# Performance work log

Measured on AMD Instinct MI355X. Metric: run time of the kernel, lower is better.

Reference implementation:

```python
import jax, jax.numpy as jnp
import numpy as np

B, T, C = 8, 2048, 1024
EXP = 4
EPS = 1e-6


def rmsnorm(x, w):
    xf = x.astype(jnp.float32)
    y = xf * jax.lax.rsqrt(jnp.mean(xf * xf, axis=-1, keepdims=True) + EPS)
    return y.astype(x.dtype) * w


def setup_inputs() -> dict:
    key = jax.random.key(0)
    ks = jax.random.split(key, 8)
    x = jax.random.normal(ks[0], (B, T, C), dtype=jnp.float32)
    norm1_w = jnp.ones((C,), jnp.float32)
    norm2_w = jnp.ones((C,), jnp.float32)
    s1 = 1.0 / np.sqrt(C)
    s2 = 1.0 / np.sqrt(EXP * C)
    mlp1_w = jax.random.uniform(ks[1], (C, C), jnp.float32, -s1, s1)  # stored (in,out)
    mlp1_b = jax.random.uniform(ks[2], (C,), jnp.float32, -s1, s1)
    mlp2_w1 = jax.random.uniform(ks[3], (C, EXP * C), jnp.float32, -s1, s1)
    mlp2_b1 = jax.random.uniform(ks[4], (EXP * C,), jnp.float32, -s1, s1)
    mlp2_w2 = jax.random.uniform(ks[5], (EXP * C, C), jnp.float32, -s2, s2)
    mlp2_b2 = jax.random.uniform(ks[6], (C,), jnp.float32, -s2, s2)
    return {"x": x, "norm1_w": norm1_w, "mlp1_w": mlp1_w, "mlp1_b": mlp1_b,
            "norm2_w": norm2_w, "mlp2_w1": mlp2_w1, "mlp2_b1": mlp2_b1,
            "mlp2_w2": mlp2_w2, "mlp2_b2": mlp2_b2}


def reference(x, norm1_w, mlp1_w, mlp1_b, norm2_w, mlp2_w1, mlp2_b1, mlp2_w2, mlp2_b2):
    Tdim = x.shape[-2]
    # linear-RNN cumulative state with triangular-number scaler (faithful to source)
    state = jnp.cumsum(rmsnorm(x, norm1_w), axis=1)
    scaler = jnp.cumsum(jnp.arange(1, Tdim + 1, dtype=x.dtype))[None, :, None]
    state = state / scaler
    gate = jax.nn.sigmoid(jnp.einsum('btc,cd->btd', state, mlp1_w) + mlp1_b)
    out = gate * x
    h = rmsnorm(out, norm2_w)
    h = jax.nn.relu(jnp.einsum('btc,ce->bte', h, mlp2_w1) + mlp2_b1)
    out = jnp.einsum('bte,ec->btc', h, mlp2_w2) + mlp2_b2 + out
    return out
```

## Files before the change

kernel.cpp:

```cpp
#include <hip/hip_runtime.h>

__device__ __forceinline__ float bf2f(unsigned short u) {
    union { unsigned int i; float f; } v;
    v.i = ((unsigned int)u) << 16;
    return v.f;
}
__device__ __forceinline__ unsigned short f2bf(float f) {
    union { float f; unsigned int i; } v;
    v.f = f;
    unsigned int r = (v.i + 0x7fffu + ((v.i >> 16) & 1u)) >> 16;
    return (unsigned short)r;
}

typedef __attribute__((ext_vector_type(8))) short short8;
typedef __attribute__((ext_vector_type(4))) float floatx4;

#define GLOBAL_AS __attribute__((address_space(1)))
#define LDS_AS __attribute__((address_space(3)))

static constexpr int Bdim = 8;
static constexpr int Tdim = 2048;
static constexpr int Cdim = 1024;
static constexpr int Edim = 4096;
static constexpr int Mdim = Bdim * Tdim;

__global__ __launch_bounds__(256) void transpose_f2b(
    const float* __restrict__ src, unsigned short* __restrict__ dst, int K, int N) {
    __shared__ float tile[32][33];
    int n0 = blockIdx.x * 32;
    int k0 = blockIdx.y * 32;
    int tx = threadIdx.x & 31;
    int ty = threadIdx.x >> 5;
#pragma unroll
    for (int i = 0; i < 32; i += 8)
        tile[ty + i][tx] = src[(size_t)(k0 + ty + i) * N + n0 + tx];
    __syncthreads();
#pragma unroll
    for (int i = 0; i < 32; i += 8)
        dst[(size_t)(n0 + ty + i) * K + k0 + tx] = f2bf(tile[tx][ty + i]);
}

__global__ __launch_bounds__(256) void rms_inv_kernel(
    const float* __restrict__ x, float* __restrict__ rinv) {
    int row = blockIdx.x;
    int tid = threadIdx.x;
    float4 v = ((const float4*)(x + (size_t)row * Cdim))[tid];
    float s = v.x * v.x + v.y * v.y + v.z * v.z + v.w * v.w;
#pragma unroll
    for (int o = 32; o > 0; o >>= 1) s += __shfl_down(s, o, 64);
    __shared__ float ps[4];
    if ((tid & 63) == 0) ps[tid >> 6] = s;
    __syncthreads();
    if (tid == 0) {
        float tot = ps[0] + ps[1] + ps[2] + ps[3];
        rinv[row] = rsqrtf(tot * (1.0f / (float)Cdim) + 1e-6f);
    }
}

__global__ __launch_bounds__(256) void chunk_sums(
    const float* __restrict__ x, const float* __restrict__ rinv,
    const float* __restrict__ w, float* __restrict__ P) {
    int idx = blockIdx.x;
    int cb = idx & 3;
    int k = (idx >> 2) & 31;
    int b = idx >> 7;
    int c = cb * 256 + threadIdx.x;
    float wc = w[c];
    const float* base = x + ((size_t)b * Tdim + k * 64) * Cdim + c;
    const float* rbase = rinv + (size_t)b * Tdim + k * 64;
    float s = 0.f;
#pragma unroll 8
    for (int t = 0; t < 64; t++) s += base[(size_t)t * Cdim] * rbase[t];
    P[((size_t)b * 32 + k) * Cdim + c] = s * wc;
}

__global__ __launch_bounds__(256) void chunk_scan(float* __restrict__ P) {
    int g = blockIdx.x * 256 + threadIdx.x;
    int b = g >> 10;
    int c = g & 1023;
    float* p = P + (size_t)b * 32 * Cdim + c;
    float run = 0.f;
#pragma unroll
    for (int k = 0; k < 32; k++) {
        float v = p[(size_t)k * Cdim];
        p[(size_t)k * Cdim] = run;
        run += v;
    }
}

__global__ __launch_bounds__(256) void cumsum_state(
    const float* __restrict__ x, const float* __restrict__ rinv,
    const float* __restrict__ w, const float* __restrict__ P,
    unsigned short* __restrict__ state) {
    int idx = blockIdx.x;
    int cb = idx & 3;
    int k = (idx >> 2) & 31;
    int b = idx >> 7;
    int c = cb * 256 + threadIdx.x;
    float wc = w[c];
    float acc = P[((size_t)b * 32 + k) * Cdim + c];
    const float* base = x + ((size_t)b * Tdim + k * 64) * Cdim + c;
    const float* rbase = rinv + (size_t)b * Tdim + k * 64;
    unsigned short* sbase = state + ((size_t)b * Tdim + k * 64) * Cdim + c;
#pragma unroll 4
    for (int t = 0; t < 64; t++) {
        acc += base[(size_t)t * Cdim] * rbase[t] * wc;
        int tt = k * 64 + t;
        float inv = 2.0f / ((float)(tt + 1) * (float)(tt + 2));
        sbase[(size_t)t * Cdim] = f2bf(acc * inv);
    }
}

__global__ __launch_bounds__(256) void rmsnorm_f2b(
    const float* __restrict__ x, const float* __restrict__ w,
    unsigned short* __restrict__ y) {
    int row = blockIdx.x;
    int tid = threadIdx.x;
    float4 v = ((const float4*)(x + (size_t)row * Cdim))[tid];
    float s = v.x * v.x + v.y * v.y + v.z * v.z + v.w * v.w;
#pragma unroll
    for (int o = 32; o > 0; o >>= 1) s += __shfl_down(s, o, 64);
    __shared__ float ps[4];
    if ((tid & 63) == 0) ps[tid >> 6] = s;
    __syncthreads();
    float tot = ps[0] + ps[1] + ps[2] + ps[3];
    float r = rsqrtf(tot * (1.0f / (float)Cdim) + 1e-6f);
    float4 w4 = ((const float4*)w)[tid];
    ushort4 o;
    o.x = f2bf(v.x * r * w4.x);
    o.y = f2bf(v.y * r * w4.y);
    o.z = f2bf(v.z * r * w4.z);
    o.w = f2bf(v.w * r * w4.w);
    ((ushort4*)(y + (size_t)row * Cdim))[tid] = o;
}

template <int EPI>
__global__ __launch_bounds__(512, 2) void gemm8(
    const unsigned short* __restrict__ A, const unsigned short* __restrict__ BT,
    const float* __restrict__ bias, const float* __restrict__ extra,
    void* __restrict__ Coutv, int N, int K) {
    __shared__ __attribute__((aligned(16))) unsigned short As[2][256 * 64];
    __shared__ __attribute__((aligned(16))) unsigned short Bs[2][256 * 64];

    int tid = threadIdx.x;
    int nbn = N >> 8;
    int id = blockIdx.x;
    int nwg = gridDim.x;
    if ((nwg & 7) == 0) id = (id & 7) * (nwg >> 3) + (id >> 3);
    int bn = id % nbn;
    int bm = id / nbn;

    int lane = tid & 63;
    int w = tid >> 6;
    int wm = w >> 2;
    int wn = w & 3;
    int lrow = lane & 15;
    int l4 = lane >> 4;
    int swz = lrow & 7;
    int wmB = wm * 128, wnB = wn * 64;

    const unsigned short* Abase = A + (size_t)bm * 256 * K;
    const unsigned short* Bbase = BT + (size_t)bn * 256 * K;

    int sr = tid >> 3;
    int col8 = (tid & 7) ^ (sr & 7);

#define STAGE_A(sb, u, k0)                                                               \
    __builtin_amdgcn_global_load_lds(                                                    \
        (const GLOBAL_AS void*)(Abase + (size_t)((u) * 64 + sr) * K + (k0) + col8 * 8),  \
        (LDS_AS void*)(As[sb] + (u) * 4096 + tid * 8), 16, 0, 0)
#define STAGE_B(sb, u, k0)                                                               \
    __builtin_amdgcn_global_load_lds(                                                    \
        (const GLOBAL_AS void*)(Bbase + (size_t)((u) * 64 + sr) * K + (k0) + col8 * 8),  \
        (LDS_AS void*)(Bs[sb] + (u) * 4096 + tid * 8), 16, 0, 0)

#define LDA(cb, i, ks)                                                                   \
    (*(const short8*)(As[cb] + (wmB + (i) * 16 + lrow) * 64 + ((((ks) * 4 + l4) ^ swz) << 3)))
#define LDB(cb, jj, ks)                                                                  \
    (*(const short8*)(Bs[cb] + (wnB + (jj) * 16 + lrow) * 64 + ((((ks) * 4 + l4) ^ swz) << 3)))

#define PH_IN                                                                            \
    do {                                                                                 \
        __builtin_amdgcn_s_barrier();                                                    \
        __builtin_amdgcn_s_setprio(1);                                                   \
    } while (0)
#define PH_OUT                                                                           \
    do {                                                                                 \
        __builtin_amdgcn_s_setprio(0);                                                   \
        __builtin_amdgcn_s_barrier();                                                    \
    } while (0)

    floatx4 acc[8][4] = {};
    int nt = K >> 6;
    int nIter = nt >> 1;

    STAGE_A(0, 0, 0); STAGE_A(0, 1, 0); STAGE_A(0, 2, 0); STAGE_A(0, 3, 0);
    STAGE_B(0, 0, 0); STAGE_B(0, 1, 0); STAGE_B(0, 2, 0); STAGE_B(0, 3, 0);
    STAGE_B(1, 0, 64); STAGE_B(1, 1, 64); STAGE_B(1, 2, 64); STAGE_B(1, 3, 64);
    asm volatile("s_waitcnt vmcnt(4)" ::: "memory");
    __builtin_amdgcn_s_barrier();

    for (int j = 0; j < nIter; ++j) {
        int k1 = (2 * j + 1) << 6;
        int k2 = (2 * j + 2) << 6;
        int k3 = (2 * j + 3) << 6;
        bool nl = (j + 1 < nIter);

        short8 av[4], b0[4], b1[4];

#pragma unroll
        for (int i = 0; i < 4; i++) av[i] = LDA(0, i, 0);
#pragma unroll
        for (int i = 0; i < 4; i++) b0[i] = LDB(0, i, 0);
        STAGE_A(1, 0, k1); STAGE_A(1, 1, k1);
        PH_IN;
#pragma unroll
        for (int i = 0; i < 4; i++)
#pragma unroll
            for (int q = 0; q < 4; q++)
                acc[i][q] = __builtin_amdgcn_mfma_f32_16x16x32_bf16(av[i], b0[q], acc[i][q], 0, 0, 0);
        PH_OUT;

#pragma unroll
        for (int i = 0; i < 4; i++) av[i] = LDA(0, i, 1);
#pragma unroll
        for (int i = 0; i < 4; i++) b1[i] = LDB(0, i, 1);
        STAGE_A(1, 2, k1); STAGE_A(1, 3, k1);
        PH_IN;
#pragma unroll
        for (int i = 0; i < 4; i++)
#pragma unroll
            for (int q = 0; q < 4; q++)
                acc[i][q] = __builtin_amdgcn_mfma_f32_16x16x32_bf16(av[i], b1[q], acc[i][q], 0, 0, 0);
        PH_OUT;

#pragma unroll
        for (int i = 0; i < 4; i++) av[i] = LDA(0, 4 + i, 0);
        if (nl) { STAGE_B(0, 0, k2); STAGE_B(0, 1, k2); }
        PH_IN;
#pragma unroll
        for (int i = 0; i < 4; i++)
#pragma unroll
            for (int q = 0; q < 4; q++)
                acc[4 + i][q] = __builtin_amdgcn_mfma_f32_16x16x32_bf16(av[i], b0[q], acc[4 + i][q], 0, 0, 0);
        PH_OUT;

#pragma unroll
        for (int i = 0; i < 4; i++) av[i] = LDA(0, 4 + i, 1);
        if (nl) { STAGE_B(0, 2, k2); STAGE_B(0, 3, k2); }
        if (nl) asm volatile("s_waitcnt vmcnt(2)" ::: "memory");
        else    asm volatile("s_waitcnt vmcnt(0)" ::: "memory");
        PH_IN;
#pragma unroll
        for (int i = 0; i < 4; i++)
#pragma unroll
            for (int q = 0; q < 4; q++)
                acc[4 + i][q] = __builtin_amdgcn_mfma_f32_16x16x32_bf16(av[i], b1[q], acc[4 + i][q], 0, 0, 0);
        PH_OUT;

#pragma unroll
        for (int i = 0; i < 4; i++) av[i] = LDA(1, i, 0);
#pragma unroll
        for (int i = 0; i < 4; i++) b0[i] = LDB(1, i, 0);
        if (nl) { STAGE_A(0, 0, k2); STAGE_A(0, 1, k2); }
        PH_IN;
#pragma unroll
        for (int i = 0; i < 4; i++)
#pragma unroll
            for (int q = 0; q < 4; q++)
                acc[i][q] = __builtin_amdgcn_mfma_f32_16x16x32_bf16(av[i], b0[q], acc[i][q], 0, 0, 0);
        PH_OUT;

#pragma unroll
        for (int i = 0; i < 4; i++) av[i] = LDA(1, i, 1);
#pragma unroll
        for (int i = 0; i < 4; i++) b1[i] = LDB(1, i, 1);
        if (nl) { STAGE_A(0, 2, k2); STAGE_A(0, 3, k2); }
        PH_IN;
#pragma unroll
        for (int i = 0; i < 4; i++)
#pragma unroll
            for (int q = 0; q < 4; q++)
                acc[i][q] = __builtin_amdgcn_mfma_f32_16x16x32_bf16(av[i], b1[q], acc[i][q], 0, 0, 0);
        PH_OUT;

#pragma unroll
        for (int i = 0; i < 4; i++) av[i] = LDA(1, 4 + i, 0);
        if (nl) { STAGE_B(1, 0, k3); STAGE_B(1, 1, k3); }
        PH_IN;
#pragma unroll
        for (int i = 0; i < 4; i++)
#pragma unroll
            for (int q = 0; q < 4; q++)
                acc[4 + i][q] = __builtin_amdgcn_mfma_f32_16x16x32_bf16(av[i], b0[q], acc[4 + i][q], 0, 0, 0);
        PH_OUT;

#pragma unroll
        for (int i = 0; i < 4; i++) av[i] = LDA(1, 4 + i, 1);
        if (nl) { STAGE_B(1, 2, k3); STAGE_B(1, 3, k3); }
        if (nl) asm volatile("s_waitcnt vmcnt(4)" ::: "memory");
        PH_IN;
#pragma unroll
        for (int i = 0; i < 4; i++)
#pragma unroll
            for (int q = 0; q < 4; q++)
                acc[4 + i][q] = __builtin_amdgcn_mfma_f32_16x16x32_bf16(av[i], b1[q], acc[4 + i][q], 0, 0, 0);
        PH_OUT;
    }
#undef STAGE_A
#undef STAGE_B
#undef LDA
#undef LDB
#undef PH_IN
#undef PH_OUT

    asm volatile("s_waitcnt vmcnt(0)" ::: "memory");

    int crow = l4 << 2;
    int ccol = lane & 15;
#pragma unroll
    for (int i = 0; i < 8; i++) {
#pragma unroll
        for (int q = 0; q < 4; q++) {
            size_t gm = (size_t)bm * 256 + wmB + i * 16 + crow;
            size_t gn = (size_t)bn * 256 + wnB + q * 16 + ccol;
            float bsv = bias[gn];
#pragma unroll
            for (int r = 0; r < 4; r++) {
                float v = acc[i][q][r] + bsv;
                size_t off = (gm + r) * (size_t)N + gn;
                if (EPI == 0) {
                    float g = 1.f / (1.f + __expf(-v));
                    ((float*)Coutv)[off] = g * extra[off];
                } else if (EPI == 1) {
                    ((unsigned short*)Coutv)[off] = f2bf(v > 0.f ? v : 0.f);
                } else {
                    ((float*)Coutv)[off] = v + extra[off];
                }
            }
        }
    }
}

extern "C" void kernel_launch(void* const* d_in, const int* in_sizes, int n_in,
                              void* d_out, int out_size, void* d_ws, size_t ws_size,
                              hipStream_t stream) {
    const float* x   = (const float*)d_in[0];
    const float* n1w = (const float*)d_in[1];
    const float* w1  = (const float*)d_in[2];
    const float* b1  = (const float*)d_in[3];
    const float* n2w = (const float*)d_in[4];
    const float* w21 = (const float*)d_in[5];
    const float* b21 = (const float*)d_in[6];
    const float* w22 = (const float*)d_in[7];
    const float* b22 = (const float*)d_in[8];
    float* out = (float*)d_out;

    char* ws = (char*)d_ws;
    const size_t MB = 1024ull * 1024ull;
    unsigned short* state = (unsigned short*)(ws);
    unsigned short* w1T   = (unsigned short*)(ws + 32 * MB);
    unsigned short* w21T  = (unsigned short*)(ws + 34 * MB);
    unsigned short* w22T  = (unsigned short*)(ws + 42 * MB);
    float* P              = (float*)(ws + 50 * MB);
    float* rinv           = (float*)(ws + 51 * MB);
    unsigned short* h     = (unsigned short*)(ws + 52 * MB);
    float* out1 = out;

    int slice_rows = Mdim;
    while (52 * MB + (size_t)slice_rows * Edim * 2 > ws_size && slice_rows > 1024)
        slice_rows >>= 1;

    transpose_f2b<<<dim3(Cdim / 32, Cdim / 32), 256, 0, stream>>>(w1, w1T, Cdim, Cdim);
    transpose_f2b<<<dim3(Edim / 32, Cdim / 32), 256, 0, stream>>>(w21, w21T, Cdim, Edim);
    transpose_f2b<<<dim3(Cdim / 32, Edim / 32), 256, 0, stream>>>(w22, w22T, Edim, Cdim);

    rms_inv_kernel<<<Mdim, 256, 0, stream>>>(x, rinv);

    chunk_sums<<<1024, 256, 0, stream>>>(x, rinv, n1w, P);
    chunk_scan<<<32, 256, 0, stream>>>(P);
    cumsum_state<<<1024, 256, 0, stream>>>(x, rinv, n1w, P, state);

    gemm8<0><<<dim3((Mdim / 256) * (Cdim / 256)), 512, 0, stream>>>(
        state, w1T, b1, x, out1, Cdim, Cdim);

    rmsnorm_f2b<<<Mdim, 256, 0, stream>>>(out1, n2w, state);

    for (int m0 = 0; m0 < Mdim; m0 += slice_rows) {
        gemm8<1><<<dim3((slice_rows / 256) * (Edim / 256)), 512, 0, stream>>>(
            state + (size_t)m0 * Cdim, w21T, b21, nullptr, h, Edim, Cdim);
        gemm8<2><<<dim3((slice_rows / 256) * (Cdim / 256)), 512, 0, stream>>>(
            h, w22T, b22, out1 + (size_t)m0 * Cdim, out + (size_t)m0 * Cdim,
            Cdim, Edim);
    }
}
```

Baseline: 559.7 us.

## Fold chunk scan into cumsum, relax vmcnt wait, use 128-tile GEMM for down-projection

```diff
diff --git a/kernel.cpp b/kernel.cpp
--- a/kernel.cpp
+++ b/kernel.cpp
@@ -74,20 +74,6 @@
     P[((size_t)b * 32 + k) * Cdim + c] = s * wc;
 }
 
-__global__ __launch_bounds__(256) void chunk_scan(float* __restrict__ P) {
-    int g = blockIdx.x * 256 + threadIdx.x;
-    int b = g >> 10;
-    int c = g & 1023;
-    float* p = P + (size_t)b * 32 * Cdim + c;
-    float run = 0.f;
-#pragma unroll
-    for (int k = 0; k < 32; k++) {
-        float v = p[(size_t)k * Cdim];
-        p[(size_t)k * Cdim] = run;
-        run += v;
-    }
-}
-
 __global__ __launch_bounds__(256) void cumsum_state(
     const float* __restrict__ x, const float* __restrict__ rinv,
     const float* __restrict__ w, const float* __restrict__ P,
@@ -98,7 +84,9 @@
     int b = idx >> 7;
     int c = cb * 256 + threadIdx.x;
     float wc = w[c];
-    float acc = P[((size_t)b * 32 + k) * Cdim + c];
+    const float* Pb = P + (size_t)b * 32 * Cdim + c;
+    float acc = 0.f;
+    for (int kk = 0; kk < k; kk++) acc += Pb[(size_t)kk * Cdim];
     const float* base = x + ((size_t)b * Tdim + k * 64) * Cdim + c;
     const float* rbase = rinv + (size_t)b * Tdim + k * 64;
     unsigned short* sbase = state + ((size_t)b * Tdim + k * 64) * Cdim + c;
@@ -248,7 +236,7 @@
 #pragma unroll
         for (int i = 0; i < 4; i++) av[i] = LDA(0, 4 + i, 1);
         if (nl) { STAGE_B(0, 2, k2); STAGE_B(0, 3, k2); }
-        if (nl) asm volatile("s_waitcnt vmcnt(2)" ::: "memory");
+        if (nl) asm volatile("s_waitcnt vmcnt(4)" ::: "memory");
         else    asm volatile("s_waitcnt vmcnt(0)" ::: "memory");
         PH_IN;
 #pragma unroll
@@ -342,6 +330,99 @@
     }
 }
 
+template <int EPI>
+__global__ __launch_bounds__(256, 3) void gemm97(
+    const unsigned short* __restrict__ A, const unsigned short* __restrict__ BT,
+    const float* __restrict__ bias, const float* __restrict__ extra,
+    void* __restrict__ Coutv, int N, int K) {
+    __shared__ __attribute__((aligned(16))) unsigned short As[2][128 * 32];
+    __shared__ __attribute__((aligned(16))) unsigned short Bs[2][128 * 32];
+
+    int tid = threadIdx.x;
+    int nbn = N >> 7;
+    int id = blockIdx.x;
+    int nwg = gridDim.x;
+    if ((nwg & 7) == 0) id = (id & 7) * (nwg >> 3) + (id >> 3);
+    int bn = id % nbn;
+    int bm = id / nbn;
+
+    int wave = tid >> 6, lane = tid & 63;
+    int wm = (wave & 1) * 64, wn = (wave >> 1) * 64;
+    int lrow = lane & 15;
+    int lk = (((lane >> 4) ^ ((lrow >> 1) & 3)) << 3);
+
+    const unsigned short* Abase = A + (size_t)bm * 128 * K;
+    const unsigned short* Bbase = BT + (size_t)bn * 128 * K;
+
+    floatx4 acc[4][4] = {};
+
+    int qrow = tid >> 2;
+    int qcol = (((tid & 3) ^ ((qrow >> 1) & 3)) << 3);
+    const unsigned short* ArowLo = Abase + (size_t)qrow * K + qcol;
+    const unsigned short* ArowHi = Abase + (size_t)(qrow + 64) * K + qcol;
+    const unsigned short* BrowLo = Bbase + (size_t)qrow * K + qcol;
+    const unsigned short* BrowHi = Bbase + (size_t)(qrow + 64) * K + qcol;
+
+#define STAGE(buf, koff)                                                                   \
+    do {                                                                                   \
+        __builtin_amdgcn_global_load_lds((const GLOBAL_AS void*)(ArowLo + (koff)),         \
+                                         (LDS_AS void*)(As[buf] + (size_t)tid * 8), 16, 0, 0); \
+        __builtin_amdgcn_global_load_lds((const GLOBAL_AS void*)(ArowHi + (koff)),         \
+                                         (LDS_AS void*)(As[buf] + (size_t)(tid + 256) * 8), 16, 0, 0); \
+        __builtin_amdgcn_global_load_lds((const GLOBAL_AS void*)(BrowLo + (koff)),         \
+                                         (LDS_AS void*)(Bs[buf] + (size_t)tid * 8), 16, 0, 0); \
+        __builtin_amdgcn_global_load_lds((const GLOBAL_AS void*)(BrowHi + (koff)),         \
+                                         (LDS_AS void*)(Bs[buf] + (size_t)(tid + 256) * 8), 16, 0, 0); \
+    } while (0)
+
+    int iters = K >> 5;
+    STAGE(0, 0);
+    for (int k = 0; k < iters; k++) {
+        int cur = k & 1;
+        __syncthreads();
+        if (k + 1 < iters) STAGE(cur ^ 1, (k + 1) << 5);
+
+        short8 af[4], bfr[4];
+#pragma unroll
+        for (int i = 0; i < 4; i++)
+            af[i] = *(const short8*)(As[cur] + (wm + i * 16 + lrow) * 32 + lk);
+#pragma unroll
+        for (int j = 0; j < 4; j++)
+            bfr[j] = *(const short8*)(Bs[cur] + (wn + j * 16 + lrow) * 32 + lk);
+#pragma unroll
+        for (int i = 0; i < 4; i++)
+#pragma unroll
+            for (int j = 0; j < 4; j++)
+                acc[i][j] = __builtin_amdgcn_mfma_f32_16x16x32_bf16(af[i], bfr[j], acc[i][j], 0, 0, 0);
+    }
+#undef STAGE
+
+    int crow = (lane >> 4) * 4;
+    int ccol = lane & 15;
+#pragma unroll
+    for (int i = 0; i < 4; i++) {
+#pragma unroll
+        for (int j = 0; j < 4; j++) {
+            size_t gm = (size_t)bm * 128 + wm + i * 16 + crow;
+            size_t gn = (size_t)bn * 128 + wn + j * 16 + ccol;
+            float bsv = bias[gn];
+#pragma unroll
+            for (int r = 0; r < 4; r++) {
+                float v = acc[i][j][r] + bsv;
+                size_t off = (gm + r) * (size_t)N + gn;
+                if (EPI == 0) {
+                    float g = 1.f / (1.f + __expf(-v));
+                    ((float*)Coutv)[off] = g * extra[off];
+                } else if (EPI == 1) {
+                    ((unsigned short*)Coutv)[off] = f2bf(v > 0.f ? v : 0.f);
+                } else {
+                    ((float*)Coutv)[off] = v + extra[off];
+                }
+            }
+        }
+    }
+}
+
 extern "C" void kernel_launch(void* const* d_in, const int* in_sizes, int n_in,
                               void* d_out, int out_size, void* d_ws, size_t ws_size,
                               hipStream_t stream) {
@@ -378,7 +459,6 @@
     rms_inv_kernel<<<Mdim, 256, 0, stream>>>(x, rinv);
 
     chunk_sums<<<1024, 256, 0, stream>>>(x, rinv, n1w, P);
-    chunk_scan<<<32, 256, 0, stream>>>(P);
     cumsum_state<<<1024, 256, 0, stream>>>(x, rinv, n1w, P, state);
 
     gemm8<0><<<dim3((Mdim / 256) * (Cdim / 256)), 512, 0, stream>>>(
@@ -389,7 +469,7 @@
     for (int m0 = 0; m0 < Mdim; m0 += slice_rows) {
         gemm8<1><<<dim3((slice_rows / 256) * (Edim / 256)), 512, 0, stream>>>(
             state + (size_t)m0 * Cdim, w21T, b21, nullptr, h, Edim, Cdim);
-        gemm8<2><<<dim3((slice_rows / 256) * (Cdim / 256)), 512, 0, stream>>>(
+        gemm97<2><<<dim3((slice_rows / 128) * (Cdim / 128)), 256, 0, stream>>>(
             h, w22T, b22, out1 + (size_t)m0 * Cdim, out + (size_t)m0 * Cdim,
             Cdim, Edim);
     }
```

New measurement: 568.8 us. About the same (+1.6%).
